# Kernel tuning notes

Measured on AMD Instinct MI355X. Metric: run time of the kernel, lower is better.

## Reference

```python
import jax, jax.numpy as jnp
import numpy as np

H = 16        # query heads
K = 4         # kv heads (GQA)
D = 128       # head_dim
HID = 2048    # hidden_size
T = 2048      # num tokens (single prefill sequence, causal)
THETA = 10000.0


def setup_inputs() -> dict:
    key = jax.random.key(0)
    k1, k2, k3 = jax.random.split(key, 3)
    hidden_states = jax.random.normal(k1, (T, HID), dtype=jnp.float32)
    position_ids = jnp.arange(T, dtype=jnp.int32)
    Wqkv = jax.random.normal(k2, (HID, (H + 2 * K) * D), dtype=jnp.float32) * 0.02
    Wo = jax.random.normal(k3, (H * D, HID), dtype=jnp.float32) * 0.02
    return {"hidden_states": hidden_states, "position_ids": position_ids,
            "Wqkv": Wqkv, "Wo": Wo}


def _rope_neox(x, pos):
    # x: [T, heads, D]; neox style: rotate halves
    half = D // 2
    inv_freq = 1.0 / (THETA ** (jnp.arange(0, D, 2, dtype=jnp.float32) / D))  # [D/2]
    ang = pos.astype(jnp.float32)[:, None] * inv_freq                          # [T, D/2]
    cos = jnp.cos(ang)[:, None, :]
    sin = jnp.sin(ang)[:, None, :]
    x1, x2 = x[..., :half], x[..., half:]
    return jnp.concatenate([x1 * cos - x2 * sin, x2 * cos + x1 * sin], axis=-1)


def reference(hidden_states, position_ids, Wqkv, Wo):
    t = hidden_states.shape[0]
    qkv = hidden_states @ Wqkv                                   # [T, (H+2K)*D]
    q = qkv[:, : H * D].reshape(t, H, D)
    k = qkv[:, H * D : (H + K) * D].reshape(t, K, D)
    v = qkv[:, (H + K) * D :].reshape(t, K, D)
    q = _rope_neox(q, position_ids)
    k = _rope_neox(k, position_ids)
    # GQA: expand kv heads to H
    rep = H // K
    k = jnp.repeat(k, rep, axis=1)                               # [T, H, D]
    v = jnp.repeat(v, rep, axis=1)
    scale = D ** -0.5
    scores = jnp.einsum('qhd,khd->hqk', q, k) * scale            # [H, T, T]
    causal = jnp.arange(t)[:, None] >= jnp.arange(t)[None, :]    # [T, T]
    scores = jnp.where(causal[None], scores, jnp.finfo(scores.dtype).min)
    probs = jax.nn.softmax(scores, axis=-1)
    ctx = jnp.einsum('hqk,khd->qhd', probs, v).reshape(t, H * D)  # [T, H*D]
    return ctx @ Wo                                              # [T, HID]
```

## Files before the change

### kernel.cpp

```cpp
#include <hip/hip_runtime.h>
#include <hip/hip_bf16.h>
#include <stdint.h>

typedef __hip_bfloat16 bf16;
typedef __attribute__((ext_vector_type(8))) short bh8;
typedef __attribute__((ext_vector_type(4))) float f32x4;

#define MFMA16(a, b, c) __builtin_amdgcn_mfma_f32_16x16x32_bf16((a), (b), (c), 0, 0, 0)

typedef const __attribute__((address_space(1))) void* gas1_t;
typedef __attribute__((address_space(3))) void* las3_t;

__device__ __forceinline__ void gload_lds16(const void* g, void* l) {
  __builtin_amdgcn_global_load_lds((gas1_t)g, (las3_t)l, 16, 0, 0);
}

__device__ __forceinline__ float bfu2f(unsigned short u) {
  union { unsigned int i; float f; } c;
  c.i = (unsigned int)u << 16;
  return c.f;
}

__global__ __launch_bounds__(256) void cast_f32_bf16(const float* __restrict__ x,
                                                     bf16* __restrict__ y, int n4) {
  int i = blockIdx.x * 256 + threadIdx.x;
  if (i >= n4) return;
  float4 v = ((const float4*)x)[i];
  union { ushort4 u; bf16 b[4]; } o;
  o.b[0] = __float2bfloat16(v.x);
  o.b[1] = __float2bfloat16(v.y);
  o.b[2] = __float2bfloat16(v.z);
  o.b[3] = __float2bfloat16(v.w);
  ((ushort4*)y)[i] = o.u;
}

__global__ __launch_bounds__(256) void transpose_cast(const float* __restrict__ W,
                                                      bf16* __restrict__ WT, int R, int C) {
  __shared__ float tile[32][33];
  const int tx = threadIdx.x & 31, ty = threadIdx.x >> 5;
  const int bx = blockIdx.x, by = blockIdx.y;
#pragma unroll
  for (int p = 0; p < 4; ++p)
    tile[ty + p * 8][tx] = W[(long)(by * 32 + ty + p * 8) * C + bx * 32 + tx];
  __syncthreads();
#pragma unroll
  for (int p = 0; p < 4; ++p)
    WT[(long)(bx * 32 + ty + p * 8) * R + by * 32 + tx] = __float2bfloat16(tile[tx][ty + p * 8]);
}

__global__ __launch_bounds__(256) void gemm_bt_sk4(const bf16* __restrict__ A,
                                                   const bf16* __restrict__ BT,
                                                   bf16* __restrict__ c0, bf16* __restrict__ c1,
                                                   bf16* __restrict__ c2, bf16* __restrict__ c3,
                                                   int M, int N, int Kd, int nKs) {
  __shared__ bf16 As[128 * 64];
  __shared__ bf16 Bs[128 * 64];
  const int tid = threadIdx.x, lane = tid & 63, wid = tid >> 6;
  const int wr = wid >> 1, wc = wid & 1;
  const int bx = blockIdx.x, by = blockIdx.y, z = blockIdx.z;

  f32x4 acc[4][4];
#pragma unroll
  for (int m = 0; m < 4; ++m)
#pragma unroll
    for (int n = 0; n < 4; ++n)
#pragma unroll
      for (int r = 0; r < 4; ++r) acc[m][n][r] = 0.0f;

  const long Abase = (long)(by * 128) * Kd;
  const long Bbase = (long)(bx * 128) * Kd;
  const int lr = lane & 15, lh = lane >> 4;
  const int k00 = z * nKs * 64;

  for (int kt = 0; kt < nKs; ++kt) {
    __syncthreads();
    const int k0 = k00 + kt * 64;
#pragma unroll
    for (int i = 0; i < 4; ++i) {
      const int cb = i * 256 + wid * 64;
      const int c = cb + lane;
      const int row = c >> 3, s = c & 7;
      gload_lds16(A + Abase + (long)row * Kd + k0 + (s ^ (row & 7)) * 8, (char*)As + cb * 16);
      gload_lds16(BT + Bbase + (long)row * Kd + k0 + (s ^ (row & 7)) * 8, (char*)Bs + cb * 16);
    }
    __syncthreads();

#pragma unroll
    for (int kk = 0; kk < 2; ++kk) {
      bh8 af[4], bfv[4];
#pragma unroll
      for (int m = 0; m < 4; ++m)
        af[m] = *(const bh8*)((const char*)As +
                              (((wr * 64 + m * 16 + lr) * 128 + kk * 64 + lh * 16) ^
                               ((lr & 7) << 4)));
#pragma unroll
      for (int n = 0; n < 4; ++n)
        bfv[n] = *(const bh8*)((const char*)Bs +
                               (((wc * 64 + n * 16 + lr) * 128 + kk * 64 + lh * 16) ^
                                ((lr & 7) << 4)));
#pragma unroll
      for (int m = 0; m < 4; ++m)
#pragma unroll
        for (int n = 0; n < 4; ++n) acc[m][n] = MFMA16(af[m], bfv[n], acc[m][n]);
    }
  }

  bf16* P = (z == 0) ? c0 : (z == 1) ? c1 : (z == 2) ? c2 : c3;
  const int r0 = by * 128 + wr * 64, c0i = bx * 128 + wc * 64;
  const int lrow = lh * 4;
#pragma unroll
  for (int m = 0; m < 4; ++m)
#pragma unroll
    for (int n = 0; n < 4; ++n)
#pragma unroll
      for (int r = 0; r < 4; ++r)
        P[(long)(r0 + m * 16 + lrow + r) * N + c0i + n * 16 + lr] =
            __float2bfloat16(acc[m][n][r]);
}

__global__ __launch_bounds__(256) void out_reduce4(float* __restrict__ out,
                                                   const bf16* __restrict__ p0,
                                                   const bf16* __restrict__ p1,
                                                   const bf16* __restrict__ p2,
                                                   const bf16* __restrict__ p3, int n8) {
  int i = blockIdx.x * 256 + threadIdx.x;
  if (i >= n8) return;
  union { bh8 v; ushort s[8]; } a, b, c, d;
  a.v = *(const bh8*)(p0 + (long)i * 8);
  b.v = *(const bh8*)(p1 + (long)i * 8);
  c.v = *(const bh8*)(p2 + (long)i * 8);
  d.v = *(const bh8*)(p3 + (long)i * 8);
  float4 o0, o1;
  float* oo = &o0.x;
#pragma unroll
  for (int e = 0; e < 8; ++e) {
    const float f = bfu2f(a.s[e]) + bfu2f(b.s[e]) + bfu2f(c.s[e]) + bfu2f(d.s[e]);
    if (e < 4) (&o0.x)[e] = f; else (&o1.x)[e - 4] = f;
  }
  (void)oo;
  ((float4*)out)[i * 2] = o0;
  ((float4*)out)[i * 2 + 1] = o1;
}

__global__ __launch_bounds__(256) void rope_split(const bf16* __restrict__ P0,
                                                  const bf16* __restrict__ P1,
                                                  const bf16* __restrict__ P2,
                                                  const bf16* __restrict__ P3,
                                                  const int* __restrict__ pos_ids,
                                                  bf16* __restrict__ Qb, bf16* __restrict__ Kb,
                                                  bf16* __restrict__ VbT) {
  __shared__ float lcs[64], lsn[64];
  const int t = blockIdx.x;
  const int tid = threadIdx.x;
  const float pos = (float)pos_ids[t];
  const float qscale = 0.08838834764831845f;
  const ushort* r0 = (const ushort*)(P0 + (long)t * 3072);
  const ushort* r1 = (const ushort*)(P1 + (long)t * 3072);
  const ushort* r2 = (const ushort*)(P2 + (long)t * 3072);
  const ushort* r3 = (const ushort*)(P3 + (long)t * 3072);

  if (tid < 64) {
    const float inv = exp2f((float)tid * -0.2076205059304594f);
    const float ang = pos * inv;
    float s, c;
    __sincosf(ang, &s, &c);
    lcs[tid] = c;
    lsn[tid] = s;
  }
  __syncthreads();

  for (int i = tid; i < 512; i += 256) {
    const int kvh = i >> 7, d = i & 127;
    const float v = bfu2f(r0[2560 + i]) + bfu2f(r1[2560 + i]) + bfu2f(r2[2560 + i]) +
                    bfu2f(r3[2560 + i]);
    VbT[(long)(kvh * 128 + d) * 2048 + t] = __float2bfloat16(v);
  }
  for (int i = tid; i < 1280; i += 256) {
    const int hh = i >> 6, d = i & 63;
    const float c = lcs[d], s = lsn[d];
    const float x1 = bfu2f(r0[hh * 128 + d]) + bfu2f(r1[hh * 128 + d]) +
                     bfu2f(r2[hh * 128 + d]) + bfu2f(r3[hh * 128 + d]);
    const float x2 = bfu2f(r0[hh * 128 + d + 64]) + bfu2f(r1[hh * 128 + d + 64]) +
                     bfu2f(r2[hh * 128 + d + 64]) + bfu2f(r3[hh * 128 + d + 64]);
    const float o1 = x1 * c - x2 * s, o2 = x2 * c + x1 * s;
    if (hh < 16) {
      Qb[(long)t * 2048 + hh * 128 + d] = __float2bfloat16(o1 * qscale);
      Qb[(long)t * 2048 + hh * 128 + d + 64] = __float2bfloat16(o2 * qscale);
    } else {
      Kb[t * 512 + (hh - 16) * 128 + d] = __float2bfloat16(o1);
      Kb[t * 512 + (hh - 16) * 128 + d + 64] = __float2bfloat16(o2);
    }
  }
}

__global__ __launch_bounds__(256, 2) void attn_partial(const bf16* __restrict__ Qb,
                                                       const bf16* __restrict__ Kb,
                                                       const bf16* __restrict__ VbT,
                                                       bf16* __restrict__ Pctx,
                                                       float* __restrict__ ML) {
  const int h = blockIdx.x;
  const int qb = 31 - blockIdx.y;
  const int z = blockIdx.z;
  const int kh = h >> 2;
  const int tid = threadIdx.x, lane = tid & 63, w = tid >> 6;
  const int pid = (h * 32 + qb) * 2 + z;

  const int nt = qb + 1;
  const int half = (nt + 1) >> 1;
  const int kt0 = z * half;
  const int kt1 = (z == 0) ? half : nt;

  if (kt0 >= kt1) {
    if (tid < 64) {
      ML[pid * 128 + tid] = -1e30f;
      ML[pid * 128 + 64 + tid] = 0.0f;
    }
    ushort4 z4 = make_ushort4(0, 0, 0, 0);
    ushort4* pz = (ushort4*)(Pctx + (long)pid * 8192);
    for (int j = tid; j < 2048; j += 256) pz[j] = z4;
    return;
  }

  __shared__ bf16 Kl[64 * 128];
  __shared__ bf16 Vt[128 * 64];

  const int lr = lane & 15, lh = lane >> 4;
  const int q0w = qb * 64 + w * 16;

  bh8 qf[4];
#pragma unroll
  for (int dc = 0; dc < 4; ++dc)
    qf[dc] = *(const bh8*)&Qb[(long)(q0w + lr) * 2048 + h * 128 + dc * 32 + lh * 8];

  f32x4 ctx[8];
#pragma unroll
  for (int i = 0; i < 8; ++i)
#pragma unroll
    for (int r = 0; r < 4; ++r) ctx[i][r] = 0.0f;
  float mrun = -1e30f, lrun = 0.0f;

  for (int kt = kt0; kt < kt1; ++kt) {
    __syncthreads();
    const long Kbase = ((long)(kt * 64) * 4 + kh) * 128;
#pragma unroll
    for (int i = 0; i < 4; ++i) {
      const int cb = i * 256 + w * 64;
      const int c = cb + lane;
      const int krow = c >> 4, s = c & 15;
      const int g = s ^ ((krow & 3) | ((krow & 8) >> 1));
      gload_lds16(Kb + Kbase + (long)krow * 512 + g * 8, (char*)Kl + cb * 16);
    }
    const long Vbase = (long)kh * 128 * 2048 + kt * 64;
#pragma unroll
    for (int i = 0; i < 4; ++i) {
      const int cb = i * 256 + w * 64;
      const int c = cb + lane;
      const int vrow = c >> 3, s = c & 7;
      gload_lds16(VbT + Vbase + (long)vrow * 2048 + (s ^ (vrow & 7)) * 8, (char*)Vt + cb * 16);
    }
    __syncthreads();

    f32x4 S[2][2];
#pragma unroll
    for (int kc = 0; kc < 2; ++kc)
#pragma unroll
      for (int b = 0; b < 2; ++b) {
#pragma unroll
        for (int r = 0; r < 4; ++r) S[kc][b][r] = 0.0f;
        const int key = kc * 32 + ((lr >> 2) << 3) + b * 4 + (lr & 3);
        const int kbase = key * 256 + lh * 16;
#pragma unroll
        for (int dc = 0; dc < 4; ++dc) {
          bh8 kf = *(const bh8*)((const char*)Kl + ((kbase + dc * 64) ^ ((lr & 7) << 4)));
          S[kc][b] = MFMA16(kf, qf[dc], S[kc][b]);
        }
      }

    if (kt == qb) {
      const int qg = q0w + lr;
#pragma unroll
      for (int kc = 0; kc < 2; ++kc)
#pragma unroll
        for (int b = 0; b < 2; ++b)
#pragma unroll
          for (int r = 0; r < 4; ++r) {
            const int kg = kt * 64 + kc * 32 + lh * 8 + b * 4 + r;
            if (kg > qg) S[kc][b][r] = -1e30f;
          }
    }

    float pm = -1e30f;
#pragma unroll
    for (int kc = 0; kc < 2; ++kc)
#pragma unroll
      for (int b = 0; b < 2; ++b)
#pragma unroll
        for (int r = 0; r < 4; ++r) pm = fmaxf(pm, S[kc][b][r]);
    pm = fmaxf(pm, __shfl_xor(pm, 16, 64));
    pm = fmaxf(pm, __shfl_xor(pm, 32, 64));

    if (__any(pm > mrun + 4.0f)) {
      const float mnew = fmaxf(mrun, pm);
      const float alpha = __expf(mrun - mnew);
      mrun = mnew;
      lrun *= alpha;
      float a4[4];
#pragma unroll
      for (int r = 0; r < 4; ++r) a4[r] = __shfl(alpha, lh * 4 + r, 64);
#pragma unroll
      for (int i = 0; i < 8; ++i)
#pragma unroll
        for (int r = 0; r < 4; ++r) ctx[i][r] *= a4[r];
    }

    bh8 pa[2];
#pragma unroll
    for (int kc = 0; kc < 2; ++kc) {
      union { bh8 v; bf16 e[8]; } pk;
#pragma unroll
      for (int b = 0; b < 2; ++b)
#pragma unroll
        for (int r = 0; r < 4; ++r) {
          const float p = __expf(S[kc][b][r] - mrun);
          lrun += p;
          pk.e[b * 4 + r] = __float2bfloat16(p);
        }
      pa[kc] = pk.v;
    }

#pragma unroll
    for (int kc = 0; kc < 2; ++kc)
#pragma unroll
      for (int dblk = 0; dblk < 8; ++dblk) {
        const int vrow = dblk * 16 + lr;
        const int voff = (vrow * 128 + kc * 64 + lh * 16) ^ ((lr & 7) << 4);
        bh8 vb = *(const bh8*)((const char*)Vt + voff);
        ctx[dblk] = MFMA16(pa[kc], vb, ctx[dblk]);
      }
  }

  float l = lrun;
  l += __shfl_xor(l, 16, 64);
  l += __shfl_xor(l, 32, 64);
  if (lh == 0) {
    ML[pid * 128 + w * 16 + lr] = mrun;
    ML[pid * 128 + 64 + w * 16 + lr] = l;
  }
#pragma unroll
  for (int dblk = 0; dblk < 8; ++dblk)
#pragma unroll
    for (int r = 0; r < 4; ++r)
      Pctx[(long)pid * 8192 + (w * 16 + lh * 4 + r) * 128 + dblk * 16 + lr] =
          __float2bfloat16(ctx[dblk][r]);
}

__global__ __launch_bounds__(256) void attn_merge(const bf16* __restrict__ Pctx,
                                                  const float* __restrict__ ML,
                                                  bf16* __restrict__ out) {
  const int h = blockIdx.x, qb = blockIdx.y;
  const int tid = threadIdx.x;
  const int r = tid >> 2, seg = tid & 3;
  const int pid0 = (h * 32 + qb) * 2;
  const float m0 = ML[pid0 * 128 + r], l0 = ML[pid0 * 128 + 64 + r];
  const float m1 = ML[pid0 * 128 + 128 + r], l1 = ML[pid0 * 128 + 192 + r];
  const float m = fmaxf(m0, m1);
  float a0 = __expf(m0 - m), a1 = __expf(m1 - m);
  const float inv = 1.0f / (l0 * a0 + l1 * a1);
  a0 *= inv;
  a1 *= inv;
  const ushort* p0 = (const ushort*)(Pctx + (long)pid0 * 8192 + r * 128 + seg * 32);
  const ushort* p1 = p0 + 8192;
  bf16* o = out + (long)(qb * 64 + r) * 2048 + h * 128 + seg * 32;
#pragma unroll
  for (int j = 0; j < 4; ++j) {
    union { bh8 v; ushort s[8]; } v0, v1;
    v0.v = *(const bh8*)(p0 + j * 8);
    v1.v = *(const bh8*)(p1 + j * 8);
    union { ushort4 u; bf16 b[4]; } o0, o1;
#pragma unroll
    for (int e = 0; e < 4; ++e) {
      o0.b[e] = __float2bfloat16(bfu2f(v0.s[e]) * a0 + bfu2f(v1.s[e]) * a1);
      o1.b[e] = __float2bfloat16(bfu2f(v0.s[e + 4]) * a0 + bfu2f(v1.s[e + 4]) * a1);
    }
    *(ushort4*)(o + j * 8) = o0.u;
    *(ushort4*)(o + j * 8 + 4) = o1.u;
  }
}

extern "C" void kernel_launch(void* const* d_in, const int* in_sizes, int n_in,
                              void* d_out, int out_size, void* d_ws, size_t ws_size,
                              hipStream_t stream) {
  const float* hs = (const float*)d_in[0];
  const int* pos = (const int*)d_in[1];
  const float* Wqkv = (const float*)d_in[2];
  const float* Wo = (const float*)d_in[3];
  char* ws = (char*)d_ws;

  bf16* hsb = (bf16*)(ws);
  bf16* ctx = (bf16*)(ws);
  bf16* wqkvT = (bf16*)(ws + (8l << 20));
  bf16* Qb = (bf16*)(ws + (8l << 20));
  bf16* Kb = (bf16*)(ws + (16l << 20));
  bf16* VbT = (bf16*)(ws + (18l << 20));
  bf16* woT = (bf16*)(ws + (20l << 20));
  bf16* qkvP0 = (bf16*)(ws + (28l << 20));
  bf16* qkvP1 = (bf16*)(ws + (40l << 20));
  bf16* qkvP2 = (bf16*)(ws + (52l << 20));
  bf16* qkvP3 = (bf16*)(ws + (64l << 20));
  bf16* Pctx = (bf16*)(ws + (28l << 20));
  float* ML = (float*)(ws + (44l << 20));
  bf16* oP0 = (bf16*)(ws + (48l << 20));
  bf16* oP1 = (bf16*)(ws + (56l << 20));
  bf16* oP2 = (bf16*)(ws + (64l << 20));
  bf16* oP3 = (bf16*)(ws + (72l << 20));

  cast_f32_bf16<<<4096, 256, 0, stream>>>(hs, hsb, 2048 * 2048 / 4);
  transpose_cast<<<dim3(3072 / 32, 2048 / 32), 256, 0, stream>>>(Wqkv, wqkvT, 2048, 3072);
  transpose_cast<<<dim3(2048 / 32, 2048 / 32), 256, 0, stream>>>(Wo, woT, 2048, 2048);
  gemm_bt_sk4<<<dim3(24, 16, 4), 256, 0, stream>>>(hsb, wqkvT, qkvP0, qkvP1, qkvP2, qkvP3,
                                                   2048, 3072, 2048, 8);
  rope_split<<<2048, 256, 0, stream>>>(qkvP0, qkvP1, qkvP2, qkvP3, pos, Qb, Kb, VbT);
  attn_partial<<<dim3(16, 32, 2), 256, 0, stream>>>(Qb, Kb, VbT, Pctx, ML);
  attn_merge<<<dim3(16, 32), 256, 0, stream>>>(Pctx, ML, ctx);
  gemm_bt_sk4<<<dim3(16, 16, 4), 256, 0, stream>>>(ctx, woT, oP0, oP1, oP2, oP3,
                                                   2048, 2048, 2048, 8);
  out_reduce4<<<2048, 256, 0, stream>>>((float*)d_out, oP0, oP1, oP2, oP3, 2048 * 2048 / 8);
}
```

Measured before the change: 232.7 us.

## Halve split-K partitions and fuse weight prep kernels into one launch

The QKV and output GEMMs now split K two ways instead of four, each slice covering 16 k-tiles. This halves the partial buffers written and read by rope_split and the output reduction. The cast of the hidden states and the two weight transposes are merged into one prep kernel, cutting launch overhead and letting the three run concurrently. Fewer k-splits mean fewer blocks per GEMM (768 and 512), which may leave the GPU underoccupied, and the output partial buffers are moved to new workspace offsets.

```diff
diff --git a/kernel.cpp b/kernel.cpp
--- a/kernel.cpp
+++ b/kernel.cpp
@@ -21,24 +21,35 @@
   return c.f;
 }
 
-__global__ __launch_bounds__(256) void cast_f32_bf16(const float* __restrict__ x,
-                                                     bf16* __restrict__ y, int n4) {
-  int i = blockIdx.x * 256 + threadIdx.x;
-  if (i >= n4) return;
-  float4 v = ((const float4*)x)[i];
-  union { ushort4 u; bf16 b[4]; } o;
-  o.b[0] = __float2bfloat16(v.x);
-  o.b[1] = __float2bfloat16(v.y);
-  o.b[2] = __float2bfloat16(v.z);
-  o.b[3] = __float2bfloat16(v.w);
-  ((ushort4*)y)[i] = o.u;
-}
-
-__global__ __launch_bounds__(256) void transpose_cast(const float* __restrict__ W,
-                                                      bf16* __restrict__ WT, int R, int C) {
+__global__ __launch_bounds__(256) void prep(const float* __restrict__ hs, bf16* __restrict__ hsb,
+                                            const float* __restrict__ Wqkv,
+                                            bf16* __restrict__ wqkvT,
+                                            const float* __restrict__ Wo,
+                                            bf16* __restrict__ woT) {
+  const int b = blockIdx.x, tid = threadIdx.x;
+  if (b < 4096) {
+    const int i = b * 256 + tid;
+    float4 v = ((const float4*)hs)[i];
+    union { ushort4 u; bf16 bb[4]; } o;
+    o.bb[0] = __float2bfloat16(v.x);
+    o.bb[1] = __float2bfloat16(v.y);
+    o.bb[2] = __float2bfloat16(v.z);
+    o.bb[3] = __float2bfloat16(v.w);
+    ((ushort4*)hsb)[i] = o.u;
+    return;
+  }
   __shared__ float tile[32][33];
-  const int tx = threadIdx.x & 31, ty = threadIdx.x >> 5;
-  const int bx = blockIdx.x, by = blockIdx.y;
+  const float* W;
+  bf16* WT;
+  int bx, by, R, C;
+  if (b < 4096 + 6144) {
+    const int bb = b - 4096;
+    bx = bb % 96; by = bb / 96; R = 2048; C = 3072; W = Wqkv; WT = wqkvT;
+  } else {
+    const int bb = b - 10240;
+    bx = bb % 64; by = bb / 64; R = 2048; C = 2048; W = Wo; WT = woT;
+  }
+  const int tx = tid & 31, ty = tid >> 5;
 #pragma unroll
   for (int p = 0; p < 4; ++p)
     tile[ty + p * 8][tx] = W[(long)(by * 32 + ty + p * 8) * C + bx * 32 + tx];
@@ -48,11 +59,10 @@
     WT[(long)(bx * 32 + ty + p * 8) * R + by * 32 + tx] = __float2bfloat16(tile[tx][ty + p * 8]);
 }
 
-__global__ __launch_bounds__(256) void gemm_bt_sk4(const bf16* __restrict__ A,
-                                                   const bf16* __restrict__ BT,
-                                                   bf16* __restrict__ c0, bf16* __restrict__ c1,
-                                                   bf16* __restrict__ c2, bf16* __restrict__ c3,
-                                                   int M, int N, int Kd, int nKs) {
+__global__ __launch_bounds__(256) void gemm_bt_sk(const bf16* __restrict__ A,
+                                                  const bf16* __restrict__ BT,
+                                                  bf16* __restrict__ C0, bf16* __restrict__ C1,
+                                                  int M, int N, int Kd, int nKs) {
   __shared__ bf16 As[128 * 64];
   __shared__ bf16 Bs[128 * 64];
   const int tid = threadIdx.x, lane = tid & 63, wid = tid >> 6;
@@ -105,7 +115,7 @@
     }
   }
 
-  bf16* P = (z == 0) ? c0 : (z == 1) ? c1 : (z == 2) ? c2 : c3;
+  bf16* P = (z == 0) ? C0 : C1;
   const int r0 = by * 128 + wr * 64, c0i = bx * 128 + wc * 64;
   const int lrow = lh * 4;
 #pragma unroll
@@ -118,34 +128,26 @@
             __float2bfloat16(acc[m][n][r]);
 }
 
-__global__ __launch_bounds__(256) void out_reduce4(float* __restrict__ out,
+__global__ __launch_bounds__(256) void out_reduce2(float* __restrict__ out,
                                                    const bf16* __restrict__ p0,
-                                                   const bf16* __restrict__ p1,
-                                                   const bf16* __restrict__ p2,
-                                                   const bf16* __restrict__ p3, int n8) {
+                                                   const bf16* __restrict__ p1, int n8) {
   int i = blockIdx.x * 256 + threadIdx.x;
   if (i >= n8) return;
-  union { bh8 v; ushort s[8]; } a, b, c, d;
+  union { bh8 v; ushort s[8]; } a, b;
   a.v = *(const bh8*)(p0 + (long)i * 8);
   b.v = *(const bh8*)(p1 + (long)i * 8);
-  c.v = *(const bh8*)(p2 + (long)i * 8);
-  d.v = *(const bh8*)(p3 + (long)i * 8);
   float4 o0, o1;
-  float* oo = &o0.x;
-#pragma unroll
-  for (int e = 0; e < 8; ++e) {
-    const float f = bfu2f(a.s[e]) + bfu2f(b.s[e]) + bfu2f(c.s[e]) + bfu2f(d.s[e]);
-    if (e < 4) (&o0.x)[e] = f; else (&o1.x)[e - 4] = f;
-  }
-  (void)oo;
+#pragma unroll
+  for (int e = 0; e < 4; ++e) {
+    (&o0.x)[e] = bfu2f(a.s[e]) + bfu2f(b.s[e]);
+    (&o1.x)[e] = bfu2f(a.s[e + 4]) + bfu2f(b.s[e + 4]);
+  }
   ((float4*)out)[i * 2] = o0;
   ((float4*)out)[i * 2 + 1] = o1;
 }
 
 __global__ __launch_bounds__(256) void rope_split(const bf16* __restrict__ P0,
                                                   const bf16* __restrict__ P1,
-                                                  const bf16* __restrict__ P2,
-                                                  const bf16* __restrict__ P3,
                                                   const int* __restrict__ pos_ids,
                                                   bf16* __restrict__ Qb, bf16* __restrict__ Kb,
                                                   bf16* __restrict__ VbT) {
@@ -156,14 +158,11 @@
   const float qscale = 0.08838834764831845f;
   const ushort* r0 = (const ushort*)(P0 + (long)t * 3072);
   const ushort* r1 = (const ushort*)(P1 + (long)t * 3072);
-  const ushort* r2 = (const ushort*)(P2 + (long)t * 3072);
-  const ushort* r3 = (const ushort*)(P3 + (long)t * 3072);
 
   if (tid < 64) {
     const float inv = exp2f((float)tid * -0.2076205059304594f);
-    const float ang = pos * inv;
     float s, c;
-    __sincosf(ang, &s, &c);
+    __sincosf(pos * inv, &s, &c);
     lcs[tid] = c;
     lsn[tid] = s;
   }
@@ -171,17 +170,14 @@
 
   for (int i = tid; i < 512; i += 256) {
     const int kvh = i >> 7, d = i & 127;
-    const float v = bfu2f(r0[2560 + i]) + bfu2f(r1[2560 + i]) + bfu2f(r2[2560 + i]) +
-                    bfu2f(r3[2560 + i]);
+    const float v = bfu2f(r0[2560 + i]) + bfu2f(r1[2560 + i]);
     VbT[(long)(kvh * 128 + d) * 2048 + t] = __float2bfloat16(v);
   }
   for (int i = tid; i < 1280; i += 256) {
     const int hh = i >> 6, d = i & 63;
     const float c = lcs[d], s = lsn[d];
-    const float x1 = bfu2f(r0[hh * 128 + d]) + bfu2f(r1[hh * 128 + d]) +
-                     bfu2f(r2[hh * 128 + d]) + bfu2f(r3[hh * 128 + d]);
-    const float x2 = bfu2f(r0[hh * 128 + d + 64]) + bfu2f(r1[hh * 128 + d + 64]) +
-                     bfu2f(r2[hh * 128 + d + 64]) + bfu2f(r3[hh * 128 + d + 64]);
+    const float x1 = bfu2f(r0[hh * 128 + d]) + bfu2f(r1[hh * 128 + d]);
+    const float x2 = bfu2f(r0[hh * 128 + d + 64]) + bfu2f(r1[hh * 128 + d + 64]);
     const float o1 = x1 * c - x2 * s, o2 = x2 * c + x1 * s;
     if (hh < 16) {
       Qb[(long)t * 2048 + hh * 128 + d] = __float2bfloat16(o1 * qscale);
@@ -405,24 +401,17 @@
   bf16* woT = (bf16*)(ws + (20l << 20));
   bf16* qkvP0 = (bf16*)(ws + (28l << 20));
   bf16* qkvP1 = (bf16*)(ws + (40l << 20));
-  bf16* qkvP2 = (bf16*)(ws + (52l << 20));
-  bf16* qkvP3 = (bf16*)(ws + (64l << 20));
   bf16* Pctx = (bf16*)(ws + (28l << 20));
   float* ML = (float*)(ws + (44l << 20));
-  bf16* oP0 = (bf16*)(ws + (48l << 20));
-  bf16* oP1 = (bf16*)(ws + (56l << 20));
-  bf16* oP2 = (bf16*)(ws + (64l << 20));
-  bf16* oP3 = (bf16*)(ws + (72l << 20));
-
-  cast_f32_bf16<<<4096, 256, 0, stream>>>(hs, hsb, 2048 * 2048 / 4);
-  transpose_cast<<<dim3(3072 / 32, 2048 / 32), 256, 0, stream>>>(Wqkv, wqkvT, 2048, 3072);
-  transpose_cast<<<dim3(2048 / 32, 2048 / 32), 256, 0, stream>>>(Wo, woT, 2048, 2048);
-  gemm_bt_sk4<<<dim3(24, 16, 4), 256, 0, stream>>>(hsb, wqkvT, qkvP0, qkvP1, qkvP2, qkvP3,
-                                                   2048, 3072, 2048, 8);
-  rope_split<<<2048, 256, 0, stream>>>(qkvP0, qkvP1, qkvP2, qkvP3, pos, Qb, Kb, VbT);
+  bf16* oP0 = (bf16*)(ws + (28l << 20));
+  bf16* oP1 = (bf16*)(ws + (36l << 20));
+
+  prep<<<14336, 256, 0, stream>>>(hs, hsb, Wqkv, wqkvT, Wo, woT);
+  gemm_bt_sk<<<dim3(24, 16, 2), 256, 0, stream>>>(hsb, wqkvT, qkvP0, qkvP1, 2048, 3072, 2048,
+                                                  16);
+  rope_split<<<2048, 256, 0, stream>>>(qkvP0, qkvP1, pos, Qb, Kb, VbT);
   attn_partial<<<dim3(16, 32, 2), 256, 0, stream>>>(Qb, Kb, VbT, Pctx, ML);
   attn_merge<<<dim3(16, 32), 256, 0, stream>>>(Pctx, ML, ctx);
-  gemm_bt_sk4<<<dim3(16, 16, 4), 256, 0, stream>>>(ctx, woT, oP0, oP1, oP2, oP3,
-                                                   2048, 2048, 2048, 8);
-  out_reduce4<<<2048, 256, 0, stream>>>((float*)d_out, oP0, oP1, oP2, oP3, 2048 * 2048 / 8);
-}
+  gemm_bt_sk<<<dim3(16, 16, 2), 256, 0, stream>>>(ctx, woT, oP0, oP1, 2048, 2048, 2048, 16);
+  out_reduce2<<<2048, 256, 0, stream>>>((float*)d_out, oP0, oP1, 2048 * 2048 / 8);
+}
```

Result: faster. 220.6 us (-5.2%).
